# Kernel optimization log

Measured on AMD Instinct MI355X. Metric: run time of the kernel, lower is better.

## Reference

```python
import jax, jax.numpy as jnp
import numpy as np

# Scatter2Operator config (matches init_kwargs)
NUM_HEADS = 16   # dims[2] / glob_size
GLOB_SIZE = 64
HEAD_SIZE = 64   # dims[2] / num_heads


def setup_inputs() -> dict:
    key = jax.random.key(0)
    ks = jax.random.split(key, 6)
    B, N, G, D0, D2 = 8, 4096, 64, 1024, 1024
    scale = 0.02
    return {
        "x0": jax.random.normal(ks[0], (B, G, D0), jnp.float32),
        "x2": jax.random.normal(ks[1], (B, N, D2), jnp.float32),
        "Wk": jax.random.normal(ks[2], (NUM_HEADS * GLOB_SIZE, D2), jnp.float32) * scale,
        "Wp": jax.random.normal(ks[3], (NUM_HEADS * HEAD_SIZE, D0), jnp.float32) * scale,
        "Wo": jax.random.normal(ks[4], (D2, NUM_HEADS * HEAD_SIZE), jnp.float32) * scale,
        "bo": jnp.zeros((D2,), jnp.float32),
    }


def reference(x0, x2, Wk, Wp, Wo, bo):
    # x2: [B, N, D2] -> kernel scores; x0: [B, G, D0] -> premise values.
    B, N, _ = x2.shape
    H, G, Dh = NUM_HEADS, GLOB_SIZE, HEAD_SIZE
    # kernel = softmax over glob slots (dropout is identity in eval mode)
    k = jnp.einsum('bnd,kd->bnk', x2, Wk).reshape(B, N, H, G)
    k = jax.nn.softmax(k, axis=-1)                      # [B, N, H, G]
    # premise projection: [B, G, H, Dh]
    p = jnp.einsum('bgd,kd->bgk', x0, Wp).reshape(B, G, H, Dh)
    # attention-like gather over the G global slots, per head
    pred = jnp.einsum('bnhg,bghd->bnhd', k, p)          # [B, N, H, Dh]
    pred = pred.reshape(B, N, H * Dh)
    # writer linear (with bias)
    return jnp.einsum('bnk,dk->bnd', pred, Wo) + bo
```

## Files before the change

kernel.cpp:

```cpp
#include <hip/hip_runtime.h>


using bf16x8 = __attribute__((ext_vector_type(8))) __bf16;
using f32x4  = __attribute__((ext_vector_type(4))) float;

__device__ __forceinline__ unsigned short f2b(float f) {
  unsigned u = __float_as_uint(f);
  u += 0x7fffu + ((u >> 16) & 1u);
  return (unsigned short)(u >> 16);
}

__global__ void cvt_all(const float* __restrict__ x2, unsigned short* __restrict__ x2b, int n0,
                        const float* __restrict__ x0, unsigned short* __restrict__ x0b, int n1,
                        const float* __restrict__ Wk, unsigned short* __restrict__ Wkb, int n2,
                        const float* __restrict__ Wp, unsigned short* __restrict__ Wpb, int n3,
                        const float* __restrict__ Wo, unsigned short* __restrict__ Wob, int n4)
{
  const int ntot = n0 + n1 + n2 + n3 + n4;
  int i = blockIdx.x * blockDim.x + threadIdx.x;
  const int stride = gridDim.x * blockDim.x;
  for (; i < ntot; i += stride) {
    const float* src; unsigned short* dst; int j = i;
    if (j < n0) { src = x2; dst = x2b; }
    else if ((j -= n0) < n1) { src = x0; dst = x0b; }
    else if ((j -= n1) < n2) { src = Wk; dst = Wkb; }
    else if ((j -= n2) < n3) { src = Wp; dst = Wpb; }
    else { j -= n3; src = Wo; dst = Wob; }
    float4 v = reinterpret_cast<const float4*>(src)[j];
    ushort4 o;
    o.x = f2b(v.x); o.y = f2b(v.y); o.z = f2b(v.z); o.w = f2b(v.w);
    reinterpret_cast<ushort4*>(dst)[j] = o;
  }
}

#define GLOAD_LDS(gsrc, ldst) __builtin_amdgcn_global_load_lds(                 \
    (const __attribute__((address_space(1))) unsigned int*)(gsrc),              \
    (__attribute__((address_space(3))) unsigned int*)(ldst), 16, 0, 0)

__device__ __forceinline__ void glds16(const unsigned short* g, unsigned ldsoff) {
  asm volatile("s_mov_b32 m0, %0\n\t"
               "global_load_lds_dwordx4 %1, off"
               :: "s"(ldsoff), "v"(g) : "memory");
}

#define BM 128
#define BN 128
#define BK 32

template<int EPI>
__launch_bounds__(256)
__global__ void gemm_bt(const unsigned short* __restrict__ A,
                        const unsigned short* __restrict__ B,
                        void* __restrict__ Cv,
                        const float* __restrict__ bias,
                        int M, int N, int K, int lda, int ldb, int ldc,
                        int batch2,
                        long sA1, long sA2, long sB1, long sB2, long sC1, long sC2)
{
  __shared__ __align__(16) unsigned short As[BM * BK];
  __shared__ __align__(16) unsigned short Bs[BN * BK];

  const int z  = blockIdx.z;
  const int z1 = z / batch2, z2 = z - z1 * batch2;
  const unsigned short* Ab = A + z1 * sA1 + z2 * sA2;
  const unsigned short* Bb = B + z1 * sB1 + z2 * sB2;
  const long cbase = z1 * sC1 + z2 * sC2;

  const int tid  = threadIdx.x;
  const int lane = tid & 63;
  const int wid  = tid >> 6;
  const int wr   = (wid >> 1) * 64;
  const int wc   = (wid & 1) * 64;
  const int brow = blockIdx.x * BM;
  const int bcol = blockIdx.y * BN;
  const int lr   = lane & 15;
  const int ko   = (lane >> 4) * 8;

  f32x4 acc[4][4] = {};

  const int t1  = tid + 256;
  const int r0  = tid >> 2, kc0 = (tid & 3) * 8;
  const int r1  = t1 >> 2,  kc1 = (t1 & 3) * 8;
  int ar0 = brow + r0; if (ar0 >= M) ar0 = M - 1;
  int ar1 = brow + r1; if (ar1 >= M) ar1 = M - 1;
  int br0 = bcol + r0; if (br0 >= N) br0 = N - 1;
  int br1 = bcol + r1; if (br1 >= N) br1 = N - 1;
  const unsigned short* a0p = Ab + (long)ar0 * lda + kc0;
  const unsigned short* a1p = Ab + (long)ar1 * lda + kc1;
  const unsigned short* b0p = Bb + (long)br0 * ldb + kc0;
  const unsigned short* b1p = Bb + (long)br1 * ldb + kc1;

  for (int kt = 0; kt < K; kt += BK) {
    __syncthreads();
    GLOAD_LDS(a0p + kt, &As[tid * 8]);
    GLOAD_LDS(a1p + kt, &As[t1 * 8]);
    GLOAD_LDS(b0p + kt, &Bs[tid * 8]);
    GLOAD_LDS(b1p + kt, &Bs[t1 * 8]);
    __syncthreads();

    bf16x8 af[4], bfr[4];
#pragma unroll
    for (int m = 0; m < 4; ++m)
      af[m] = *reinterpret_cast<const bf16x8*>(&As[(wr + m * 16 + lr) * BK + ko]);
#pragma unroll
    for (int n = 0; n < 4; ++n)
      bfr[n] = *reinterpret_cast<const bf16x8*>(&Bs[(wc + n * 16 + lr) * BK + ko]);
#pragma unroll
    for (int m = 0; m < 4; ++m)
#pragma unroll
      for (int n = 0; n < 4; ++n)
        acc[m][n] = __builtin_amdgcn_mfma_f32_16x16x32_bf16(af[m], bfr[n], acc[m][n], 0, 0, 0);
  }

  const int rowb = brow + wr + (lane >> 4) * 4;
  const int colb = bcol + wc + lr;

  if (EPI == 1) {
    float* C = (float*)Cv + cbase;
#pragma unroll
    for (int n = 0; n < 4; ++n) {
      int col = colb + n * 16;
      if (col >= N) continue;
      float bv = bias ? bias[col] : 0.0f;
#pragma unroll
      for (int m = 0; m < 4; ++m)
#pragma unroll
        for (int r = 0; r < 4; ++r) {
          int row = rowb + m * 16 + r;
          if (row < M) C[(long)row * ldc + col] = acc[m][n][r] + bv;
        }
    }
  } else {
    unsigned short* C = (unsigned short*)Cv + cbase;
#pragma unroll
    for (int n = 0; n < 4; ++n) {
      int col = colb + n * 16;
      if (col >= N) continue;
#pragma unroll
      for (int m = 0; m < 4; ++m)
#pragma unroll
        for (int r = 0; r < 4; ++r) {
          int row = rowb + m * 16 + r;
          if (row < M) C[(long)row * ldc + col] = f2b(acc[m][n][r]);
        }
    }
  }
}


#define BARRIER() __builtin_amdgcn_s_barrier()
#define VMC4()   asm volatile("s_waitcnt vmcnt(4)" ::: "memory")
#define VMC0()   asm volatile("s_waitcnt vmcnt(0)" ::: "memory")

template<int EPI, int BATCHED>
__launch_bounds__(512)
__global__ void gemm256(const unsigned short* __restrict__ A,
                        const unsigned short* __restrict__ B,
                        void* __restrict__ Cv,
                        const float* __restrict__ bias,
                        int K, int lda, int ldb, int ldc,
                        long sA, long sB, long sC)
{
  extern __shared__ __align__(16) char smem[];

  const int tid  = threadIdx.x;
  const int lane = tid & 63, wid = tid >> 6;
  const int wm = wid >> 2, wn = wid & 3;
  const int lr = lane & 15, hi = lane >> 4;
  const int swz  = (lane & 7) << 4;
  const int prow = lane >> 3;
  const int pxor = ((lane & 7) ^ prow) * 8;

  int bx, by; long abase = 0, bbase = 0, cbase = 0;
  if (BATCHED) {
    const int bid = blockIdx.x;
    const int z = bid & 7, idx = bid >> 3;
    bx = idx & 15; by = idx >> 4;
    abase = (long)z * sA; bbase = (long)z * sB; cbase = (long)z * sC;
  } else {
    const int bid = blockIdx.x;
    const int lin = (bid & 7) * 64 + (bid >> 3);
    bx = lin >> 2; by = lin & 3;
  }
  const int brow = bx * 256, bcol = by * 256;

  const unsigned short* __restrict__ Ab = A + abase;
  const unsigned short* __restrict__ Bb = B + bbase;

  unsigned short* ldsA[2] = { (unsigned short*)(smem),
                              (unsigned short*)(smem + 65536) };
  unsigned short* ldsB[2] = { (unsigned short*)(smem + 32768),
                              (unsigned short*)(smem + 98304) };

  const unsigned ldsbase =
      __builtin_amdgcn_readfirstlane((unsigned)(unsigned long long)smem);

  const long ldaL = lda, ldbL = ldb;

  auto stageA = [&](int buf, int h, int kt) {
    const unsigned short* s = Ab + (long)(brow + h * 128 + wid * 8 + prow) * ldaL + kt + pxor;
    unsigned d = ldsbase + (unsigned)(buf * 65536 + h * 16384 + wid * 1024);
    glds16(s, __builtin_amdgcn_readfirstlane(d));
    glds16(s + 64 * ldaL, __builtin_amdgcn_readfirstlane(d + 8192u));
  };
  auto stageB = [&](int buf, int h, int kt) {
    const unsigned short* s = Bb + (long)(bcol + h * 128 + wid * 8 + prow) * ldbL + kt + pxor;
    unsigned d = ldsbase + (unsigned)(32768 + buf * 65536 + h * 16384 + wid * 1024);
    glds16(s, __builtin_amdgcn_readfirstlane(d));
    glds16(s + 64 * ldbL, __builtin_amdgcn_readfirstlane(d + 8192u));
  };

  bf16x8 afr[4][2], bfr[4][2];
  auto ldA_ = [&](int buf, int mh) {
    const unsigned short* base = ldsA[buf];
#pragma unroll
    for (int mi = 0; mi < 4; ++mi) {
      const int row = wm * 128 + mh * 64 + mi * 16 + lr;
#pragma unroll
      for (int ks = 0; ks < 2; ++ks) {
        const int cb = (ks * 64 + hi * 16) ^ swz;
        afr[mi][ks] = *(const bf16x8*)(base + row * 64 + (cb >> 1));
      }
    }
  };
  auto ldB_ = [&](int buf, int nh) {
    const unsigned short* base = ldsB[buf];
#pragma unroll
    for (int ni = 0; ni < 2; ++ni) {
      const int row = wn * 64 + nh * 32 + ni * 16 + lr;
#pragma unroll
      for (int ks = 0; ks < 2; ++ks) {
        const int cb = (ks * 64 + hi * 16) ^ swz;
        bfr[nh * 2 + ni][ks] = *(const bf16x8*)(base + row * 64 + (cb >> 1));
      }
    }
  };

  f32x4 acc[8][4] = {};
  auto mmaQ = [&](int mh, int nh) {
    __builtin_amdgcn_s_setprio(1);
#pragma unroll
    for (int ks = 0; ks < 2; ++ks)
#pragma unroll
      for (int mi = 0; mi < 4; ++mi)
#pragma unroll
        for (int ni = 0; ni < 2; ++ni)
          acc[mh * 4 + mi][nh * 2 + ni] = __builtin_amdgcn_mfma_f32_16x16x32_bf16(
              afr[mi][ks], bfr[nh * 2 + ni][ks], acc[mh * 4 + mi][nh * 2 + ni], 0, 0, 0);
    __builtin_amdgcn_s_setprio(0);
  };

  stageB(0, 0, 0); stageB(0, 1, 0); stageA(0, 0, 0); stageA(0, 1, 0);
  stageB(1, 0, 64); stageB(1, 1, 64);
  VMC4(); BARRIER();

  const int NI = K >> 7;
#pragma unroll 1
  for (int i = 0; i < NI; ++i) {
    const int kt1 = i * 128 + 64;
    int kt2 = i * 128 + 128; if (kt2 >= K) kt2 -= K;
    int kt3 = i * 128 + 192; if (kt3 >= K) kt3 -= K;

    ldA_(0, 0); ldB_(0, 0); ldB_(0, 1); stageA(1, 0, kt1);
    BARRIER(); mmaQ(0, 0); BARRIER();
    stageA(1, 1, kt1);
    BARRIER(); mmaQ(0, 1); BARRIER();
    ldA_(0, 1); stageB(0, 0, kt2);
    BARRIER(); mmaQ(1, 0); BARRIER();
    stageB(0, 1, kt2); VMC4();
    BARRIER(); mmaQ(1, 1); BARRIER();
    ldA_(1, 0); ldB_(1, 0); ldB_(1, 1); stageA(0, 0, kt2);
    BARRIER(); mmaQ(0, 0); BARRIER();
    stageA(0, 1, kt2);
    BARRIER(); mmaQ(0, 1); BARRIER();
    ldA_(1, 1); stageB(1, 0, kt3);
    BARRIER(); mmaQ(1, 0); BARRIER();
    stageB(1, 1, kt3); VMC4();
    BARRIER(); mmaQ(1, 1); BARRIER();
  }
  VMC0();

  const int rowb = brow + wm * 128 + hi * 4;
  const int colb = bcol + wn * 64 + lr;

  if (EPI == 2) {
    unsigned short* C = (unsigned short*)Cv + cbase;
#pragma unroll
    for (int m = 0; m < 8; ++m) {
#pragma unroll
      for (int r = 0; r < 4; ++r) {
        float v0 = acc[m][0][r], v1 = acc[m][1][r], v2 = acc[m][2][r], v3 = acc[m][3][r];
        float mx = fmaxf(fmaxf(v0, v1), fmaxf(v2, v3));
        mx = fmaxf(mx, __shfl_xor(mx, 1));
        mx = fmaxf(mx, __shfl_xor(mx, 2));
        mx = fmaxf(mx, __shfl_xor(mx, 4));
        mx = fmaxf(mx, __shfl_xor(mx, 8));
        float e0 = __expf(v0 - mx), e1 = __expf(v1 - mx);
        float e2 = __expf(v2 - mx), e3 = __expf(v3 - mx);
        float s = e0 + e1 + e2 + e3;
        s += __shfl_xor(s, 1);
        s += __shfl_xor(s, 2);
        s += __shfl_xor(s, 4);
        s += __shfl_xor(s, 8);
        float inv = 1.0f / s;
        unsigned short* cp = C + (long)(rowb + m * 16 + r) * ldc + colb;
        cp[0]  = f2b(e0 * inv);
        cp[16] = f2b(e1 * inv);
        cp[32] = f2b(e2 * inv);
        cp[48] = f2b(e3 * inv);
      }
    }
  } else {
    float* C = (float*)Cv + cbase;
#pragma unroll
    for (int n = 0; n < 4; ++n) {
      const int col = colb + n * 16;
      const float bv = bias[col];
#pragma unroll
      for (int m = 0; m < 8; ++m)
#pragma unroll
        for (int r = 0; r < 4; ++r)
          C[(long)(rowb + m * 16 + r) * ldc + col] = acc[m][n][r] + bv;
    }
  }
}

extern "C" void kernel_launch(void* const* d_in, const int* in_sizes, int n_in,
                              void* d_out, int out_size, void* d_ws, size_t ws_size,
                              hipStream_t stream) {
  (void)in_sizes; (void)n_in; (void)out_size; (void)ws_size;
  const float* x0 = (const float*)d_in[0];
  const float* x2 = (const float*)d_in[1];
  const float* Wk = (const float*)d_in[2];
  const float* Wp = (const float*)d_in[3];
  const float* Wo = (const float*)d_in[4];
  const float* bo = (const float*)d_in[5];
  float* out = (float*)d_out;

  const long Bz = 8, Nn = 4096, Gg = 64, Dd = 1024;
  const long MN = Bz * Nn;

  char* ws = (char*)d_ws;
  size_t off = 0;
  auto alloc = [&](size_t bytes) {
    size_t cur = off;
    off = (cur + bytes + 255) & ~(size_t)255;
    return (unsigned short*)(ws + cur);
  };
  unsigned short* x2b = alloc(MN * Dd * 2);
  unsigned short* kb  = alloc(MN * Dd * 2);
  unsigned short* Wkb = alloc(Dd * Dd * 2);
  unsigned short* Wpb = alloc(Dd * Dd * 2);
  unsigned short* Wob = alloc(Dd * Dd * 2);
  unsigned short* x0b = alloc(Bz * Gg * Dd * 2);
  unsigned short* Pb  = alloc(Bz * Gg * Dd * 2);
  unsigned short* Qtb = alloc(Bz * Dd * Dd * 2);

  hipFuncSetAttribute(reinterpret_cast<const void*>(gemm256<2, 0>),
                      hipFuncAttributeMaxDynamicSharedMemorySize, 131072);
  hipFuncSetAttribute(reinterpret_cast<const void*>(gemm256<1, 1>),
                      hipFuncAttributeMaxDynamicSharedMemorySize, 131072);

  cvt_all<<<dim3(4096), dim3(256), 0, stream>>>(
      x2, x2b, (int)(MN * Dd / 4),
      x0, x0b, (int)(Bz * Gg * Dd / 4),
      Wk, Wkb, (int)(Dd * Dd / 4),
      Wp, Wpb, (int)(Dd * Dd / 4),
      Wo, Wob, (int)(Dd * Dd / 4));

  gemm_bt<0><<<dim3(4, 8, 1), dim3(256), 0, stream>>>(
      x0b, Wpb, Pb, nullptr, 512, 1024, 1024, 1024, 1024, 1024,
      1, 0, 0, 0, 0, 0, 0);

  gemm256<2, 0><<<dim3(512, 1, 1), dim3(512), 131072, stream>>>(
      x2b, Wkb, kb, nullptr, 1024, 1024, 1024, 1024, 0, 0, 0);

  gemm_bt<0><<<dim3(8, 1, 128), dim3(256), 0, stream>>>(
      Wob, Pb, Qtb, nullptr, 1024, 64, 64, 1024, 1024, 1024,
      16, 0, 64, 65536, 64, 1048576, 64);

  gemm256<1, 1><<<dim3(512, 1, 1), dim3(512), 131072, stream>>>(
      kb, Qtb, (void*)out, bo, 1024, 1024, 1024, 1024,
      (long)4096 * 1024, (long)1024 * 1024, (long)4096 * 1024);
}
```

Before: 245.7 us.

## Double-buffer MFMA fragment registers to prefetch LDS reads ahead of MMAs

Splits the A and B fragment registers into separate buffers so the LDS reads for the next quarter-tile are issued before the current quarter's MFMAs, instead of immediately before them. Global-to-LDS staging is regrouped into pairs with the wait placed accordingly, and the prologue now preloads the first fragments. The goal is to hide LDS read latency behind matrix math. The cost is higher register pressure and a more delicate buffer and barrier ordering that has to stay race-free.

```diff
diff --git a/kernel.cpp b/kernel.cpp
--- a/kernel.cpp
+++ b/kernel.cpp
@@ -210,8 +210,10 @@
     glds16(s + 64 * ldbL, __builtin_amdgcn_readfirstlane(d + 8192u));
   };
 
-  bf16x8 afr[4][2], bfr[4][2];
-  auto ldA_ = [&](int buf, int mh) {
+  bf16x8 afr0[4][2], afr1[4][2];
+  bf16x8 bloA[2][2], bloB[2][2], bhi[2][2];
+
+  auto ldA = [&](int buf, int mh, bf16x8 (&dst)[4][2]) {
     const unsigned short* base = ldsA[buf];
 #pragma unroll
     for (int mi = 0; mi < 4; ++mi) {
@@ -219,11 +221,11 @@
 #pragma unroll
       for (int ks = 0; ks < 2; ++ks) {
         const int cb = (ks * 64 + hi * 16) ^ swz;
-        afr[mi][ks] = *(const bf16x8*)(base + row * 64 + (cb >> 1));
+        dst[mi][ks] = *(const bf16x8*)(base + row * 64 + (cb >> 1));
       }
     }
   };
-  auto ldB_ = [&](int buf, int nh) {
+  auto ldB = [&](int buf, int nh, bf16x8 (&dst)[2][2]) {
     const unsigned short* base = ldsB[buf];
 #pragma unroll
     for (int ni = 0; ni < 2; ++ni) {
@@ -231,13 +233,13 @@
 #pragma unroll
       for (int ks = 0; ks < 2; ++ks) {
         const int cb = (ks * 64 + hi * 16) ^ swz;
-        bfr[nh * 2 + ni][ks] = *(const bf16x8*)(base + row * 64 + (cb >> 1));
+        dst[ni][ks] = *(const bf16x8*)(base + row * 64 + (cb >> 1));
       }
     }
   };
 
   f32x4 acc[8][4] = {};
-  auto mmaQ = [&](int mh, int nh) {
+  auto mma = [&](bf16x8 (&a)[4][2], bf16x8 (&b)[2][2], int mh, int nh) {
     __builtin_amdgcn_s_setprio(1);
 #pragma unroll
     for (int ks = 0; ks < 2; ++ks)
@@ -246,13 +248,14 @@
 #pragma unroll
         for (int ni = 0; ni < 2; ++ni)
           acc[mh * 4 + mi][nh * 2 + ni] = __builtin_amdgcn_mfma_f32_16x16x32_bf16(
-              afr[mi][ks], bfr[nh * 2 + ni][ks], acc[mh * 4 + mi][nh * 2 + ni], 0, 0, 0);
+              a[mi][ks], b[ni][ks], acc[mh * 4 + mi][nh * 2 + ni], 0, 0, 0);
     __builtin_amdgcn_s_setprio(0);
   };
 
-  stageB(0, 0, 0); stageB(0, 1, 0); stageA(0, 0, 0); stageA(0, 1, 0);
+  stageA(0, 0, 0); stageA(0, 1, 0); stageB(0, 0, 0); stageB(0, 1, 0);
   stageB(1, 0, 64); stageB(1, 1, 64);
-  VMC4(); BARRIER();
+  VMC0(); BARRIER();
+  ldA(0, 0, afr0); ldB(0, 0, bloA);
 
   const int NI = K >> 7;
 #pragma unroll 1
@@ -261,22 +264,26 @@
     int kt2 = i * 128 + 128; if (kt2 >= K) kt2 -= K;
     int kt3 = i * 128 + 192; if (kt3 >= K) kt3 -= K;
 
-    ldA_(0, 0); ldB_(0, 0); ldB_(0, 1); stageA(1, 0, kt1);
-    BARRIER(); mmaQ(0, 0); BARRIER();
-    stageA(1, 1, kt1);
-    BARRIER(); mmaQ(0, 1); BARRIER();
-    ldA_(0, 1); stageB(0, 0, kt2);
-    BARRIER(); mmaQ(1, 0); BARRIER();
-    stageB(0, 1, kt2); VMC4();
-    BARRIER(); mmaQ(1, 1); BARRIER();
-    ldA_(1, 0); ldB_(1, 0); ldB_(1, 1); stageA(0, 0, kt2);
-    BARRIER(); mmaQ(0, 0); BARRIER();
-    stageA(0, 1, kt2);
-    BARRIER(); mmaQ(0, 1); BARRIER();
-    ldA_(1, 1); stageB(1, 0, kt3);
-    BARRIER(); mmaQ(1, 0); BARRIER();
-    stageB(1, 1, kt3); VMC4();
-    BARRIER(); mmaQ(1, 1); BARRIER();
+    ldB(0, 1, bhi);
+    stageA(1, 0, kt1); stageA(1, 1, kt1); VMC4();
+    BARRIER(); mma(afr0, bloA, 0, 0); BARRIER();
+    ldA(0, 1, afr1);
+    BARRIER(); mma(afr0, bhi, 0, 1); BARRIER();
+    ldB(1, 0, bloB);
+    stageB(0, 0, kt2); stageB(0, 1, kt2); VMC4();
+    BARRIER(); mma(afr1, bloA, 1, 0); BARRIER();
+    ldA(1, 0, afr0);
+    BARRIER(); mma(afr1, bhi, 1, 1); BARRIER();
+    ldB(1, 1, bhi);
+    stageA(0, 0, kt2); stageA(0, 1, kt2); VMC4();
+    BARRIER(); mma(afr0, bloB, 0, 0); BARRIER();
+    ldA(1, 1, afr1);
+    BARRIER(); mma(afr0, bhi, 0, 1); BARRIER();
+    ldB(0, 0, bloA);
+    stageB(1, 0, kt3); stageB(1, 1, kt3); VMC4();
+    BARRIER(); mma(afr1, bloB, 1, 0); BARRIER();
+    ldA(0, 0, afr0);
+    BARRIER(); mma(afr1, bhi, 1, 1); BARRIER();
   }
   VMC0();
 
```

Result: slower. 289.1 us (+17.7%).

## Fuse fp32-to-bf16 conversion of x2 into the score GEMM A-operand load

Applied to the files above, without the earlier changes.

Removes the separate bf16 conversion pass over the large x2 activation. The score GEMM now loads fp32 A tiles straight into registers, converts them with packed bf16 instructions and writes them into swizzled LDS, while B still goes through direct global-to-LDS loads. This saves a full read and write of x2 in bf16 and drops one workspace buffer. In exchange the A path uses more registers and needs register-staged conversion inside the pipeline, which may reduce overlap.

```diff
diff --git a/kernel.cpp b/kernel.cpp
--- a/kernel.cpp
+++ b/kernel.cpp
@@ -10,19 +10,17 @@
   return (unsigned short)(u >> 16);
 }
 
-__global__ void cvt_all(const float* __restrict__ x2, unsigned short* __restrict__ x2b, int n0,
-                        const float* __restrict__ x0, unsigned short* __restrict__ x0b, int n1,
-                        const float* __restrict__ Wk, unsigned short* __restrict__ Wkb, int n2,
-                        const float* __restrict__ Wp, unsigned short* __restrict__ Wpb, int n3,
-                        const float* __restrict__ Wo, unsigned short* __restrict__ Wob, int n4)
+__global__ void cvt_small(const float* __restrict__ x0, unsigned short* __restrict__ x0b, int n1,
+                          const float* __restrict__ Wk, unsigned short* __restrict__ Wkb, int n2,
+                          const float* __restrict__ Wp, unsigned short* __restrict__ Wpb, int n3,
+                          const float* __restrict__ Wo, unsigned short* __restrict__ Wob, int n4)
 {
-  const int ntot = n0 + n1 + n2 + n3 + n4;
+  const int ntot = n1 + n2 + n3 + n4;
   int i = blockIdx.x * blockDim.x + threadIdx.x;
   const int stride = gridDim.x * blockDim.x;
   for (; i < ntot; i += stride) {
     const float* src; unsigned short* dst; int j = i;
-    if (j < n0) { src = x2; dst = x2b; }
-    else if ((j -= n0) < n1) { src = x0; dst = x0b; }
+    if (j < n1) { src = x0; dst = x0b; }
     else if ((j -= n1) < n2) { src = Wk; dst = Wkb; }
     else if ((j -= n2) < n3) { src = Wp; dst = Wpb; }
     else { j -= n3; src = Wo; dst = Wob; }
@@ -147,10 +145,11 @@
   }
 }
 
-
 #define BARRIER() __builtin_amdgcn_s_barrier()
 #define VMC4()   asm volatile("s_waitcnt vmcnt(4)" ::: "memory")
+#define VMC8()   asm volatile("s_waitcnt vmcnt(8)" ::: "memory")
 #define VMC0()   asm volatile("s_waitcnt vmcnt(0)" ::: "memory")
+#define LGKM0()  asm volatile("s_waitcnt lgkmcnt(0)" ::: "memory")
 
 template<int EPI, int BATCHED>
 __launch_bounds__(512)
@@ -325,6 +324,178 @@
   }
 }
 
+__launch_bounds__(512)
+__global__ void gemm256_af32(const float* __restrict__ A,
+                             const unsigned short* __restrict__ B,
+                             unsigned short* __restrict__ Cb,
+                             int K, int lda, int ldb, int ldc)
+{
+  extern __shared__ __align__(16) char smem[];
+
+  const int tid  = threadIdx.x;
+  const int lane = tid & 63, wid = tid >> 6;
+  const int wm = wid >> 2, wn = wid & 3;
+  const int lr = lane & 15, hi = lane >> 4;
+  const int swz  = (lane & 7) << 4;
+  const int prow = lane >> 3;
+  const int pxor = ((lane & 7) ^ prow) * 8;
+
+  const int bid = blockIdx.x;
+  const int lin = (bid & 7) * 64 + (bid >> 3);
+  const int bx = lin >> 2, by = lin & 3;
+  const int brow = bx * 256, bcol = by * 256;
+
+  unsigned short* ldsA[2] = { (unsigned short*)(smem),
+                              (unsigned short*)(smem + 65536) };
+  unsigned short* ldsB[2] = { (unsigned short*)(smem + 32768),
+                              (unsigned short*)(smem + 98304) };
+  const unsigned ldsbase =
+      __builtin_amdgcn_readfirstlane((unsigned)(unsigned long long)smem);
+
+  const long ldaL = lda, ldbL = ldb;
+
+  auto stageB = [&](int buf, int h, int kt) {
+    const unsigned short* s = B + (long)(bcol + h * 128 + wid * 8 + prow) * ldbL + kt + pxor;
+    unsigned d = ldsbase + (unsigned)(32768 + buf * 65536 + h * 16384 + wid * 1024);
+    glds16(s, __builtin_amdgcn_readfirstlane(d));
+    glds16(s + 64 * ldbL, __builtin_amdgcn_readfirstlane(d + 8192u));
+  };
+
+  const float* aBase = A + (long)(brow + wid * 8 + prow) * ldaL + (lane & 7) * 8;
+  float4 ar[8];
+  auto gloadA = [&](int kt) {
+#pragma unroll
+    for (int j = 0; j < 4; ++j) {
+      const float* p = aBase + kt + (long)j * 64 * ldaL;
+      asm volatile("global_load_dwordx4 %0, %1, off" : "=v"(ar[j * 2]) : "v"(p) : "memory");
+      asm volatile("global_load_dwordx4 %0, %1, off offset:16" : "=v"(ar[j * 2 + 1]) : "v"(p) : "memory");
+    }
+  };
+  auto cvtwriteA = [&](int buf) {
+    unsigned short* dA = ldsA[buf];
+    const int chunk = ((lane & 7) ^ prow) * 8;
+#pragma unroll
+    for (int j = 0; j < 4; ++j) {
+      unsigned w0, w1, w2, w3;
+      asm volatile("v_cvt_pk_bf16_f32 %0, %1, %2" : "=v"(w0) : "v"(ar[j*2].x),   "v"(ar[j*2].y));
+      asm volatile("v_cvt_pk_bf16_f32 %0, %1, %2" : "=v"(w1) : "v"(ar[j*2].z),   "v"(ar[j*2].w));
+      asm volatile("v_cvt_pk_bf16_f32 %0, %1, %2" : "=v"(w2) : "v"(ar[j*2+1].x), "v"(ar[j*2+1].y));
+      asm volatile("v_cvt_pk_bf16_f32 %0, %1, %2" : "=v"(w3) : "v"(ar[j*2+1].w), "v"(ar[j*2+1].w));
+      asm volatile("v_cvt_pk_bf16_f32 %0, %1, %2" : "=v"(w3) : "v"(ar[j*2+1].z), "v"(ar[j*2+1].w));
+      const int h = j >> 1;
+      const int rl = wid * 8 + prow + (j & 1) * 64;
+      uint4 v; v.x = w0; v.y = w1; v.z = w2; v.w = w3;
+      *(uint4*)(dA + h * 8192 + rl * 64 + chunk) = v;
+    }
+  };
+
+  bf16x8 afr[4][2], bfr[4][2];
+  auto ldA_ = [&](int buf, int mh) {
+    const unsigned short* base = ldsA[buf];
+#pragma unroll
+    for (int mi = 0; mi < 4; ++mi) {
+      const int row = wm * 128 + mh * 64 + mi * 16 + lr;
+#pragma unroll
+      for (int ks = 0; ks < 2; ++ks) {
+        const int cb = (ks * 64 + hi * 16) ^ swz;
+        afr[mi][ks] = *(const bf16x8*)(base + row * 64 + (cb >> 1));
+      }
+    }
+  };
+  auto ldB_ = [&](int buf, int nh) {
+    const unsigned short* base = ldsB[buf];
+#pragma unroll
+    for (int ni = 0; ni < 2; ++ni) {
+      const int row = wn * 64 + nh * 32 + ni * 16 + lr;
+#pragma unroll
+      for (int ks = 0; ks < 2; ++ks) {
+        const int cb = (ks * 64 + hi * 16) ^ swz;
+        bfr[nh * 2 + ni][ks] = *(const bf16x8*)(base + row * 64 + (cb >> 1));
+      }
+    }
+  };
+
+  f32x4 acc[8][4] = {};
+  auto mmaQ = [&](int mh, int nh) {
+    __builtin_amdgcn_s_setprio(1);
+#pragma unroll
+    for (int ks = 0; ks < 2; ++ks)
+#pragma unroll
+      for (int mi = 0; mi < 4; ++mi)
+#pragma unroll
+        for (int ni = 0; ni < 2; ++ni)
+          acc[mh * 4 + mi][nh * 2 + ni] = __builtin_amdgcn_mfma_f32_16x16x32_bf16(
+              afr[mi][ks], bfr[nh * 2 + ni][ks], acc[mh * 4 + mi][nh * 2 + ni], 0, 0, 0);
+    __builtin_amdgcn_s_setprio(0);
+  };
+
+  gloadA(0);
+  stageB(0, 0, 0); stageB(0, 1, 0);
+  stageB(1, 0, 64); stageB(1, 1, 64);
+  VMC8(); __builtin_amdgcn_sched_barrier(0);
+  cvtwriteA(0);
+  VMC4(); LGKM0(); BARRIER();
+
+  const int NI = K >> 7;
+#pragma unroll 1
+  for (int i = 0; i < NI; ++i) {
+    const int kt1 = i * 128 + 64;
+    int kt2 = i * 128 + 128; if (kt2 >= K) kt2 -= K;
+    int kt3 = i * 128 + 192; if (kt3 >= K) kt3 -= K;
+
+    ldA_(0, 0); ldB_(0, 0); ldB_(0, 1); gloadA(kt1);
+    BARRIER(); mmaQ(0, 0); BARRIER();
+    BARRIER(); mmaQ(0, 1); BARRIER();
+    ldA_(0, 1);
+    VMC0(); __builtin_amdgcn_sched_barrier(0);
+    cvtwriteA(1);
+    stageB(0, 0, kt2); stageB(0, 1, kt2);
+    LGKM0();
+    BARRIER(); mmaQ(1, 0); BARRIER();
+    BARRIER(); mmaQ(1, 1); BARRIER();
+    ldA_(1, 0); ldB_(1, 0); ldB_(1, 1); gloadA(kt2);
+    BARRIER(); mmaQ(0, 0); BARRIER();
+    BARRIER(); mmaQ(0, 1); BARRIER();
+    ldA_(1, 1);
+    VMC0(); __builtin_amdgcn_sched_barrier(0);
+    cvtwriteA(0);
+    stageB(1, 0, kt3); stageB(1, 1, kt3);
+    LGKM0();
+    BARRIER(); mmaQ(1, 0); BARRIER();
+    BARRIER(); mmaQ(1, 1); BARRIER();
+  }
+  VMC0();
+
+  const int rowb = brow + wm * 128 + hi * 4;
+  const int colb = bcol + wn * 64 + lr;
+  unsigned short* C = Cb;
+#pragma unroll
+  for (int m = 0; m < 8; ++m) {
+#pragma unroll
+    for (int r = 0; r < 4; ++r) {
+      float v0 = acc[m][0][r], v1 = acc[m][1][r], v2 = acc[m][2][r], v3 = acc[m][3][r];
+      float mx = fmaxf(fmaxf(v0, v1), fmaxf(v2, v3));
+      mx = fmaxf(mx, __shfl_xor(mx, 1));
+      mx = fmaxf(mx, __shfl_xor(mx, 2));
+      mx = fmaxf(mx, __shfl_xor(mx, 4));
+      mx = fmaxf(mx, __shfl_xor(mx, 8));
+      float e0 = __expf(v0 - mx), e1 = __expf(v1 - mx);
+      float e2 = __expf(v2 - mx), e3 = __expf(v3 - mx);
+      float s = e0 + e1 + e2 + e3;
+      s += __shfl_xor(s, 1);
+      s += __shfl_xor(s, 2);
+      s += __shfl_xor(s, 4);
+      s += __shfl_xor(s, 8);
+      float inv = 1.0f / s;
+      unsigned short* cp = C + (long)(rowb + m * 16 + r) * ldc + colb;
+      cp[0]  = f2b(e0 * inv);
+      cp[16] = f2b(e1 * inv);
+      cp[32] = f2b(e2 * inv);
+      cp[48] = f2b(e3 * inv);
+    }
+  }
+}
+
 extern "C" void kernel_launch(void* const* d_in, const int* in_sizes, int n_in,
                               void* d_out, int out_size, void* d_ws, size_t ws_size,
                               hipStream_t stream) {
@@ -347,7 +518,6 @@
     off = (cur + bytes + 255) & ~(size_t)255;
     return (unsigned short*)(ws + cur);
   };
-  unsigned short* x2b = alloc(MN * Dd * 2);
   unsigned short* kb  = alloc(MN * Dd * 2);
   unsigned short* Wkb = alloc(Dd * Dd * 2);
   unsigned short* Wpb = alloc(Dd * Dd * 2);
@@ -356,13 +526,12 @@
   unsigned short* Pb  = alloc(Bz * Gg * Dd * 2);
   unsigned short* Qtb = alloc(Bz * Dd * Dd * 2);
 
-  hipFuncSetAttribute(reinterpret_cast<const void*>(gemm256<2, 0>),
+  hipFuncSetAttribute(reinterpret_cast<const void*>(gemm256_af32),
                       hipFuncAttributeMaxDynamicSharedMemorySize, 131072);
   hipFuncSetAttribute(reinterpret_cast<const void*>(gemm256<1, 1>),
                       hipFuncAttributeMaxDynamicSharedMemorySize, 131072);
 
-  cvt_all<<<dim3(4096), dim3(256), 0, stream>>>(
-      x2, x2b, (int)(MN * Dd / 4),
+  cvt_small<<<dim3(1024), dim3(256), 0, stream>>>(
       x0, x0b, (int)(Bz * Gg * Dd / 4),
       Wk, Wkb, (int)(Dd * Dd / 4),
       Wp, Wpb, (int)(Dd * Dd / 4),
@@ -372,8 +541,8 @@
       x0b, Wpb, Pb, nullptr, 512, 1024, 1024, 1024, 1024, 1024,
       1, 0, 0, 0, 0, 0, 0);
 
-  gemm256<2, 0><<<dim3(512, 1, 1), dim3(512), 131072, stream>>>(
-      x2b, Wkb, kb, nullptr, 1024, 1024, 1024, 1024, 0, 0, 0);
+  gemm256_af32<<<dim3(512, 1, 1), dim3(512), 131072, stream>>>(
+      x2, Wkb, kb, 1024, 1024, 1024, 1024);
 
   gemm_bt<0><<<dim3(8, 1, 128), dim3(256), 0, stream>>>(
       Wob, Pb, Qtb, nullptr, 1024, 64, 64, 1024, 1024, 1024,
```

After: 252.3 us. 2.7% more time.
